# Optimization experiments

Measured on AMD Instinct MI355X. Metric: run time of the kernel, lower is better.

Reference implementation:

```python
import jax, jax.numpy as jnp
import numpy as np

N_NODES = 100000
N_EDGES = 1600000
N_AGENTS = 50000
D_X, D_LSTM, D_Z, D_EDGE = 64, 64, 32, 48
D_IN = D_X + D_LSTM + D_Z + D_EDGE  # 208
D_HID, D_OUT = 256, 64


def setup_inputs() -> dict:
    key = jax.random.key(0)
    ks = jax.random.split(key, 10)
    x = jax.random.normal(ks[0], (N_NODES, D_X), dtype=jnp.float32)
    x_lstm = jax.random.normal(ks[1], (N_AGENTS, D_LSTM), dtype=jnp.float32)
    encoded_z_gnss = jax.random.normal(ks[2], (N_AGENTS, D_Z), dtype=jnp.float32)
    edge_index = jax.random.randint(ks[3], (2, N_EDGES), 0, N_NODES, dtype=jnp.int64)
    edge_attr = jax.random.normal(ks[4], (N_EDGES, D_EDGE), dtype=jnp.float32)
    node_idx = jax.random.randint(ks[5], (N_AGENTS,), 0, N_NODES, dtype=jnp.int64)
    # MLP params (node_mlp: Linear(208,256) -> ReLU -> Linear(256,64))
    W1 = jax.random.normal(ks[6], (D_IN, D_HID), dtype=jnp.float32) * (1.0 / np.sqrt(D_IN))
    b1 = jnp.zeros((D_HID,), dtype=jnp.float32)
    W2 = jax.random.normal(ks[7], (D_HID, D_OUT), dtype=jnp.float32) * (1.0 / np.sqrt(D_HID))
    b2 = jnp.zeros((D_OUT,), dtype=jnp.float32)
    return {"x": x, "x_lstm": x_lstm, "encoded_z_gnss": encoded_z_gnss,
            "edge_index": edge_index, "edge_attr": edge_attr,
            "node_indexes_related_to_agent": node_idx,
            "W1": W1, "b1": b1, "W2": W2, "b2": b2}


def reference(x, x_lstm, encoded_z_gnss, edge_index, edge_attr,
              node_indexes_related_to_agent, W1, b1, W2, b2):
    row = edge_index[0]
    # node_agg_fn: scatter-sum edge features into source nodes -> [N, D_EDGE]
    agg = jax.ops.segment_sum(edge_attr, row, num_segments=x.shape[0])
    idx = node_indexes_related_to_agent
    # gather + concat -> [A, D_IN]
    out = jnp.concatenate([x[idx], x_lstm, encoded_z_gnss, agg[idx]], axis=1)
    # node_mlp
    h = jax.nn.relu(out @ W1 + b1)
    return h @ W2 + b2
```

## Files before the change

### kernel.cpp

```cpp
#include <hip/hip_runtime.h>

#define N_NODES  100000
#define N_EDGES  1600000
#define N_AGENTS 50000
#define D_EDGE   48
#define D_IN     208
#define D_HID    256
#define D_OUT    64

#define K1_PAD   224
#define F_STRIDE 248
#define H_STRIDE 264
#define AGB      64

#define BCAP     64

typedef __attribute__((ext_vector_type(8))) short short8;
typedef __attribute__((ext_vector_type(4))) float f32x4;

static __device__ __forceinline__ unsigned short f2bf(float f) {
    unsigned u = __float_as_uint(f);
    u += 0x7FFFu + ((u >> 16) & 1u);
    return (unsigned short)(u >> 16);
}

__global__ __launch_bounds__(256)
void prep_w(const float* __restrict__ W1, const float* __restrict__ W2,
            unsigned short* __restrict__ w1p, unsigned short* __restrict__ w2p) {
    int t = blockIdx.x * 256 + threadIdx.x;
    if (t < 16 * 7 * 64) {
        int lane = t & 63;
        int ks   = (t >> 6) % 7;
        int tile = t / (7 * 64);
        int n = tile * 16 + (lane & 15);
        int kb = ks * 32 + (lane >> 4) * 8;
        unsigned short v[8];
        #pragma unroll
        for (int j = 0; j < 8; ++j) {
            int k = kb + j;
            v[j] = (k < D_IN) ? f2bf(W1[k * D_HID + n]) : (unsigned short)0;
        }
        #pragma unroll
        for (int j = 0; j < 8; ++j) w1p[t * 8 + j] = v[j];
    } else if (t < 16 * 7 * 64 + 4 * 8 * 64) {
        int u = t - 16 * 7 * 64;
        int lane = u & 63;
        int ks   = (u >> 6) & 7;
        int tile = u / (8 * 64);
        int o = tile * 16 + (lane & 15);
        int kb = ks * 32 + (lane >> 4) * 8;
        #pragma unroll
        for (int j = 0; j < 8; ++j)
            w2p[u * 8 + j] = f2bf(W2[(kb + j) * D_OUT + o]);
    }
}

__global__ __launch_bounds__(256)
void mask_kernel(const int* __restrict__ node_idx, int* __restrict__ mask) {
    int i = blockIdx.x * 256 + threadIdx.x;
    if (i < N_AGENTS) mask[node_idx[i]] = 1;
}

__global__ __launch_bounds__(256)
void place_kernel(const int* __restrict__ row, const int* __restrict__ mask,
                  int* __restrict__ cnt, int* __restrict__ bucket) {
    int e = blockIdx.x * 256 + threadIdx.x;
    if (e >= N_EDGES) return;
    int r = row[e];
    if (!mask[r]) return;
    int pos = atomicAdd(&cnt[r], 1);
    if (pos < BCAP) bucket[r * BCAP + pos] = e;
}

__global__ __launch_bounds__(256)
void gather_kernel(const float* __restrict__ edge_attr,
                   const int* __restrict__ mask, const int* __restrict__ cnt,
                   const int* __restrict__ bucket,
                   float* __restrict__ agg) {
    int gid = blockIdx.x * 256 + threadIdx.x;
    if (gid >= N_NODES * D_EDGE) return;
    int n = gid / D_EDGE;
    int c = gid - n * D_EDGE;
    if (!mask[n]) return;
    int deg = cnt[n];
    if (deg > BCAP) deg = BCAP;
    const int* brow = &bucket[n * BCAP];
    float acc = 0.f;
    int j = 0;
    for (; j + 4 <= deg; j += 4) {
        int e0 = brow[j + 0];
        int e1 = brow[j + 1];
        int e2 = brow[j + 2];
        int e3 = brow[j + 3];
        float a0 = edge_attr[(long long)e0 * D_EDGE + c];
        float a1 = edge_attr[(long long)e1 * D_EDGE + c];
        float a2 = edge_attr[(long long)e2 * D_EDGE + c];
        float a3 = edge_attr[(long long)e3 * D_EDGE + c];
        acc += (a0 + a1) + (a2 + a3);
    }
    for (; j < deg; ++j) {
        int e0 = brow[j];
        acc += edge_attr[(long long)e0 * D_EDGE + c];
    }
    agg[(long long)n * D_EDGE + c] = acc;
}

__global__ __launch_bounds__(256)
void mlp_mfma(const float* __restrict__ x,
              const float* __restrict__ x_lstm,
              const float* __restrict__ z,
              const float* __restrict__ agg,
              const int* __restrict__ node_idx,
              const unsigned short* __restrict__ w1p,
              const float* __restrict__ b1,
              const unsigned short* __restrict__ w2p,
              const float* __restrict__ b2,
              float* __restrict__ out) {
    __shared__ unsigned short feat[AGB][F_STRIDE];
    __shared__ unsigned short hbuf[AGB][H_STRIDE];

    const int tid  = threadIdx.x;
    const int w    = tid >> 6;
    const int lane = tid & 63;
    const int ag0  = blockIdx.x * AGB;

    {
        const int a   = tid >> 2;
        const int sub = tid & 3;
        const int ag  = ag0 + a;
        unsigned short* frow = &feat[a][0];
        if (ag < N_AGENTS) {
            const int nid = node_idx[ag];
            #pragma unroll
            for (int i = 0; i < 4; ++i) {
                int q = i * 4 + sub;
                float4 v = *reinterpret_cast<const float4*>(&x[(long long)nid * 64 + q * 4]);
                ushort4 b; b.x = f2bf(v.x); b.y = f2bf(v.y); b.z = f2bf(v.z); b.w = f2bf(v.w);
                *reinterpret_cast<ushort4*>(&frow[q * 4]) = b;
            }
            #pragma unroll
            for (int i = 0; i < 4; ++i) {
                int q = i * 4 + sub;
                float4 v = *reinterpret_cast<const float4*>(&x_lstm[(long long)ag * 64 + q * 4]);
                ushort4 b; b.x = f2bf(v.x); b.y = f2bf(v.y); b.z = f2bf(v.z); b.w = f2bf(v.w);
                *reinterpret_cast<ushort4*>(&frow[64 + q * 4]) = b;
            }
            #pragma unroll
            for (int i = 0; i < 2; ++i) {
                int q = i * 4 + sub;
                float4 v = *reinterpret_cast<const float4*>(&z[(long long)ag * 32 + q * 4]);
                ushort4 b; b.x = f2bf(v.x); b.y = f2bf(v.y); b.z = f2bf(v.z); b.w = f2bf(v.w);
                *reinterpret_cast<ushort4*>(&frow[128 + q * 4]) = b;
            }
            #pragma unroll
            for (int i = 0; i < 3; ++i) {
                int q = i * 4 + sub;
                float4 v = *reinterpret_cast<const float4*>(&agg[(long long)nid * D_EDGE + q * 4]);
                ushort4 b; b.x = f2bf(v.x); b.y = f2bf(v.y); b.z = f2bf(v.z); b.w = f2bf(v.w);
                *reinterpret_cast<ushort4*>(&frow[160 + q * 4]) = b;
            }
            ushort4 zz; zz.x = 0; zz.y = 0; zz.z = 0; zz.w = 0;
            *reinterpret_cast<ushort4*>(&frow[208 + sub * 4]) = zz;
        } else {
            ushort4 zz; zz.x = 0; zz.y = 0; zz.z = 0; zz.w = 0;
            #pragma unroll
            for (int i = 0; i < 14; ++i)
                *reinterpret_cast<ushort4*>(&frow[(i * 4 + sub) * 4]) = zz;
        }
    }
    __syncthreads();

    const int m16 = lane & 15;
    const int g   = lane >> 4;

    const short8* w1v = reinterpret_cast<const short8*>(w1p);
    const short8* w2v = reinterpret_cast<const short8*>(w2p);

    for (int mc = 0; mc < 2; ++mc) {
        const int a0 = mc * 32 + m16;
        const int a1 = mc * 32 + 16 + m16;
        short8 bf0[7], bf1[7];
        #pragma unroll
        for (int ks = 0; ks < 7; ++ks) {
            bf0[ks] = *reinterpret_cast<const short8*>(&feat[a0][ks * 32 + g * 8]);
            bf1[ks] = *reinterpret_cast<const short8*>(&feat[a1][ks * 32 + g * 8]);
        }
        #pragma unroll
        for (int nt = 0; nt < 4; ++nt) {
            const int gt = w * 4 + nt;
            f32x4 c0 = {0.f, 0.f, 0.f, 0.f};
            f32x4 c1 = {0.f, 0.f, 0.f, 0.f};
            #pragma unroll
            for (int ks = 0; ks < 7; ++ks) {
                short8 wf = w1v[(gt * 7 + ks) * 64 + lane];
                c0 = __builtin_amdgcn_mfma_f32_16x16x32_bf16(wf, bf0[ks], c0, 0, 0, 0);
                c1 = __builtin_amdgcn_mfma_f32_16x16x32_bf16(wf, bf1[ks], c1, 0, 0, 0);
            }
            float4 bb = *reinterpret_cast<const float4*>(&b1[gt * 16 + g * 4]);
            ushort4 h0, h1;
            h0.x = f2bf(fmaxf(c0[0] + bb.x, 0.f));
            h0.y = f2bf(fmaxf(c0[1] + bb.y, 0.f));
            h0.z = f2bf(fmaxf(c0[2] + bb.z, 0.f));
            h0.w = f2bf(fmaxf(c0[3] + bb.w, 0.f));
            h1.x = f2bf(fmaxf(c1[0] + bb.x, 0.f));
            h1.y = f2bf(fmaxf(c1[1] + bb.y, 0.f));
            h1.z = f2bf(fmaxf(c1[2] + bb.z, 0.f));
            h1.w = f2bf(fmaxf(c1[3] + bb.w, 0.f));
            *reinterpret_cast<ushort4*>(&hbuf[a0][gt * 16 + g * 4]) = h0;
            *reinterpret_cast<ushort4*>(&hbuf[a1][gt * 16 + g * 4]) = h1;
        }
    }
    __syncthreads();

    {
        short8 w2f[8];
        #pragma unroll
        for (int ks = 0; ks < 8; ++ks)
            w2f[ks] = w2v[(w * 8 + ks) * 64 + lane];

        float4 bo = *reinterpret_cast<const float4*>(&b2[w * 16 + g * 4]);
        #pragma unroll
        for (int mt = 0; mt < 4; ++mt) {
            const int a = mt * 16 + m16;
            short8 hf[8];
            #pragma unroll
            for (int ks = 0; ks < 8; ++ks)
                hf[ks] = *reinterpret_cast<const short8*>(&hbuf[a][ks * 32 + g * 8]);
            f32x4 acc = {0.f, 0.f, 0.f, 0.f};
            #pragma unroll
            for (int ks = 0; ks < 8; ++ks)
                acc = __builtin_amdgcn_mfma_f32_16x16x32_bf16(w2f[ks], hf[ks], acc, 0, 0, 0);
            const int ag = ag0 + a;
            if (ag < N_AGENTS) {
                float4 o4;
                o4.x = acc[0] + bo.x;
                o4.y = acc[1] + bo.y;
                o4.z = acc[2] + bo.z;
                o4.w = acc[3] + bo.w;
                *reinterpret_cast<float4*>(&out[(long long)ag * D_OUT + w * 16 + g * 4]) = o4;
            }
        }
    }
}

extern "C" void kernel_launch(void* const* d_in, const int* in_sizes, int n_in,
                              void* d_out, int out_size, void* d_ws, size_t ws_size,
                              hipStream_t stream) {
    const float* x        = (const float*)d_in[0];
    const float* x_lstm   = (const float*)d_in[1];
    const float* z        = (const float*)d_in[2];
    const int*   edge_idx = (const int*)d_in[3];
    const float* edge_attr= (const float*)d_in[4];
    const int*   node_idx = (const int*)d_in[5];
    const float* W1       = (const float*)d_in[6];
    const float* b1       = (const float*)d_in[7];
    const float* W2       = (const float*)d_in[8];
    const float* b2       = (const float*)d_in[9];
    float* out = (float*)d_out;

    char* wsp = (char*)d_ws;
    size_t o = 0;
    auto alloc = [&](size_t bytes) { char* p = wsp + o; o = (o + bytes + 255) & ~(size_t)255; return p; };
    float* agg  = (float*)alloc((size_t)N_NODES * D_EDGE * 4);
    int* cnt    = (int*)alloc((size_t)N_NODES * 4);
    int* mask   = (int*)alloc((size_t)N_NODES * 4);
    int* bucket = (int*)alloc((size_t)N_NODES * BCAP * 4);
    unsigned short* w1p = (unsigned short*)alloc((size_t)16 * 7 * 64 * 8 * 2);
    unsigned short* w2p = (unsigned short*)alloc((size_t)4 * 8 * 64 * 8 * 2);

    hipMemsetAsync(cnt, 0, (size_t)((char*)bucket - (char*)cnt), stream);

    prep_w<<<(16 * 7 * 64 + 4 * 8 * 64 + 255) / 256, 256, 0, stream>>>(W1, W2, w1p, w2p);
    mask_kernel<<<(N_AGENTS + 255) / 256, 256, 0, stream>>>(node_idx, mask);
    place_kernel<<<(N_EDGES + 255) / 256, 256, 0, stream>>>(edge_idx, mask, cnt, bucket);
    gather_kernel<<<(N_NODES * D_EDGE + 255) / 256, 256, 0, stream>>>(
        edge_attr, mask, cnt, bucket, agg);
    mlp_mfma<<<(N_AGENTS + AGB - 1) / AGB, 256, 0, stream>>>(x, x_lstm, z, agg, node_idx,
                                                             w1p, b1, w2p, b2, out);
}
```

Before: 114.6 us.

## Fuse edge aggregation into MLP kernel and merge memset into weight prep

Drops the separate gather kernel and the agg buffer. Each agent's feature-load threads now sum their node's bucketed edge rows directly, with float4 loads, before converting to bf16. The hipMemsetAsync of cnt and mask is folded into the weight-prep kernel as extra zeroing blocks, which removes a launch and the agg write/read round trip. The cost is more irregular gather work inside the MLP kernel, and duplicate node indices now redo the same aggregation.

```diff
diff --git a/kernel.cpp b/kernel.cpp
--- a/kernel.cpp
+++ b/kernel.cpp
@@ -14,6 +14,8 @@
 #define AGB      64
 
 #define BCAP     64
+#define PREP_BLOCKS 36
+#define ZERO_INT4   50016
 
 typedef __attribute__((ext_vector_type(8))) short short8;
 typedef __attribute__((ext_vector_type(4))) float f32x4;
@@ -25,33 +27,43 @@
 }
 
 __global__ __launch_bounds__(256)
-void prep_w(const float* __restrict__ W1, const float* __restrict__ W2,
-            unsigned short* __restrict__ w1p, unsigned short* __restrict__ w2p) {
-    int t = blockIdx.x * 256 + threadIdx.x;
-    if (t < 16 * 7 * 64) {
-        int lane = t & 63;
-        int ks   = (t >> 6) % 7;
-        int tile = t / (7 * 64);
-        int n = tile * 16 + (lane & 15);
-        int kb = ks * 32 + (lane >> 4) * 8;
-        unsigned short v[8];
-        #pragma unroll
-        for (int j = 0; j < 8; ++j) {
-            int k = kb + j;
-            v[j] = (k < D_IN) ? f2bf(W1[k * D_HID + n]) : (unsigned short)0;
-        }
-        #pragma unroll
-        for (int j = 0; j < 8; ++j) w1p[t * 8 + j] = v[j];
-    } else if (t < 16 * 7 * 64 + 4 * 8 * 64) {
-        int u = t - 16 * 7 * 64;
-        int lane = u & 63;
-        int ks   = (u >> 6) & 7;
-        int tile = u / (8 * 64);
-        int o = tile * 16 + (lane & 15);
-        int kb = ks * 32 + (lane >> 4) * 8;
-        #pragma unroll
-        for (int j = 0; j < 8; ++j)
-            w2p[u * 8 + j] = f2bf(W2[(kb + j) * D_OUT + o]);
+void prep0(const float* __restrict__ W1, const float* __restrict__ W2,
+           unsigned short* __restrict__ w1p, unsigned short* __restrict__ w2p,
+           int4* __restrict__ zbase) {
+    const int b = blockIdx.x;
+    if (b < PREP_BLOCKS) {
+        int t = b * 256 + threadIdx.x;
+        if (t < 16 * 7 * 64) {
+            int lane = t & 63;
+            int ks   = (t >> 6) % 7;
+            int tile = t / (7 * 64);
+            int n = tile * 16 + (lane & 15);
+            int kb = ks * 32 + (lane >> 4) * 8;
+            unsigned short v[8];
+            #pragma unroll
+            for (int j = 0; j < 8; ++j) {
+                int k = kb + j;
+                v[j] = (k < D_IN) ? f2bf(W1[k * D_HID + n]) : (unsigned short)0;
+            }
+            #pragma unroll
+            for (int j = 0; j < 8; ++j) w1p[t * 8 + j] = v[j];
+        } else if (t < 16 * 7 * 64 + 4 * 8 * 64) {
+            int u = t - 16 * 7 * 64;
+            int lane = u & 63;
+            int ks   = (u >> 6) & 7;
+            int tile = u / (8 * 64);
+            int o = tile * 16 + (lane & 15);
+            int kb = ks * 32 + (lane >> 4) * 8;
+            #pragma unroll
+            for (int j = 0; j < 8; ++j)
+                w2p[u * 8 + j] = f2bf(W2[(kb + j) * D_OUT + o]);
+        }
+    } else {
+        int i = (b - PREP_BLOCKS) * 256 + threadIdx.x;
+        if (i < ZERO_INT4) {
+            int4 zz; zz.x = 0; zz.y = 0; zz.z = 0; zz.w = 0;
+            zbase[i] = zz;
+        }
     }
 }
 
@@ -69,47 +81,16 @@
     int r = row[e];
     if (!mask[r]) return;
     int pos = atomicAdd(&cnt[r], 1);
-    if (pos < BCAP) bucket[r * BCAP + pos] = e;
-}
-
-__global__ __launch_bounds__(256)
-void gather_kernel(const float* __restrict__ edge_attr,
-                   const int* __restrict__ mask, const int* __restrict__ cnt,
-                   const int* __restrict__ bucket,
-                   float* __restrict__ agg) {
-    int gid = blockIdx.x * 256 + threadIdx.x;
-    if (gid >= N_NODES * D_EDGE) return;
-    int n = gid / D_EDGE;
-    int c = gid - n * D_EDGE;
-    if (!mask[n]) return;
-    int deg = cnt[n];
-    if (deg > BCAP) deg = BCAP;
-    const int* brow = &bucket[n * BCAP];
-    float acc = 0.f;
-    int j = 0;
-    for (; j + 4 <= deg; j += 4) {
-        int e0 = brow[j + 0];
-        int e1 = brow[j + 1];
-        int e2 = brow[j + 2];
-        int e3 = brow[j + 3];
-        float a0 = edge_attr[(long long)e0 * D_EDGE + c];
-        float a1 = edge_attr[(long long)e1 * D_EDGE + c];
-        float a2 = edge_attr[(long long)e2 * D_EDGE + c];
-        float a3 = edge_attr[(long long)e3 * D_EDGE + c];
-        acc += (a0 + a1) + (a2 + a3);
-    }
-    for (; j < deg; ++j) {
-        int e0 = brow[j];
-        acc += edge_attr[(long long)e0 * D_EDGE + c];
-    }
-    agg[(long long)n * D_EDGE + c] = acc;
+    if ((unsigned)pos < (unsigned)BCAP) bucket[r * BCAP + pos] = e;
 }
 
 __global__ __launch_bounds__(256)
 void mlp_mfma(const float* __restrict__ x,
               const float* __restrict__ x_lstm,
               const float* __restrict__ z,
-              const float* __restrict__ agg,
+              const float* __restrict__ edge_attr,
+              const int* __restrict__ cnt,
+              const int* __restrict__ bucket,
               const int* __restrict__ node_idx,
               const unsigned short* __restrict__ w1p,
               const float* __restrict__ b1,
@@ -152,12 +133,47 @@
                 ushort4 b; b.x = f2bf(v.x); b.y = f2bf(v.y); b.z = f2bf(v.z); b.w = f2bf(v.w);
                 *reinterpret_cast<ushort4*>(&frow[128 + q * 4]) = b;
             }
-            #pragma unroll
-            for (int i = 0; i < 3; ++i) {
-                int q = i * 4 + sub;
-                float4 v = *reinterpret_cast<const float4*>(&agg[(long long)nid * D_EDGE + q * 4]);
-                ushort4 b; b.x = f2bf(v.x); b.y = f2bf(v.y); b.z = f2bf(v.z); b.w = f2bf(v.w);
-                *reinterpret_cast<ushort4*>(&frow[160 + q * 4]) = b;
+            {
+                int deg = cnt[nid];
+                if (deg > BCAP) deg = BCAP;
+                const int* brow = &bucket[nid * BCAP];
+                const float* ea = edge_attr + sub * 12;
+                float acc[12];
+                #pragma unroll
+                for (int q = 0; q < 12; ++q) acc[q] = 0.f;
+                int j = 0;
+                for (; j + 2 <= deg; j += 2) {
+                    const float* p0 = ea + (long long)brow[j] * D_EDGE;
+                    const float* p1 = ea + (long long)brow[j + 1] * D_EDGE;
+                    float4 a0 = *reinterpret_cast<const float4*>(p0);
+                    float4 a1 = *reinterpret_cast<const float4*>(p0 + 4);
+                    float4 a2 = *reinterpret_cast<const float4*>(p0 + 8);
+                    float4 c0 = *reinterpret_cast<const float4*>(p1);
+                    float4 c1 = *reinterpret_cast<const float4*>(p1 + 4);
+                    float4 c2 = *reinterpret_cast<const float4*>(p1 + 8);
+                    acc[0] += a0.x; acc[1] += a0.y; acc[2]  += a0.z; acc[3]  += a0.w;
+                    acc[4] += a1.x; acc[5] += a1.y; acc[6]  += a1.z; acc[7]  += a1.w;
+                    acc[8] += a2.x; acc[9] += a2.y; acc[10] += a2.z; acc[11] += a2.w;
+                    acc[0] += c0.x; acc[1] += c0.y; acc[2]  += c0.z; acc[3]  += c0.w;
+                    acc[4] += c1.x; acc[5] += c1.y; acc[6]  += c1.z; acc[7]  += c1.w;
+                    acc[8] += c2.x; acc[9] += c2.y; acc[10] += c2.z; acc[11] += c2.w;
+                }
+                if (j < deg) {
+                    const float* p0 = ea + (long long)brow[j] * D_EDGE;
+                    float4 a0 = *reinterpret_cast<const float4*>(p0);
+                    float4 a1 = *reinterpret_cast<const float4*>(p0 + 4);
+                    float4 a2 = *reinterpret_cast<const float4*>(p0 + 8);
+                    acc[0] += a0.x; acc[1] += a0.y; acc[2]  += a0.z; acc[3]  += a0.w;
+                    acc[4] += a1.x; acc[5] += a1.y; acc[6]  += a1.z; acc[7]  += a1.w;
+                    acc[8] += a2.x; acc[9] += a2.y; acc[10] += a2.z; acc[11] += a2.w;
+                }
+                ushort4 u0, u1, u2;
+                u0.x = f2bf(acc[0]); u0.y = f2bf(acc[1]); u0.z = f2bf(acc[2]);  u0.w = f2bf(acc[3]);
+                u1.x = f2bf(acc[4]); u1.y = f2bf(acc[5]); u1.z = f2bf(acc[6]);  u1.w = f2bf(acc[7]);
+                u2.x = f2bf(acc[8]); u2.y = f2bf(acc[9]); u2.z = f2bf(acc[10]); u2.w = f2bf(acc[11]);
+                *reinterpret_cast<ushort4*>(&frow[160 + sub * 12])     = u0;
+                *reinterpret_cast<ushort4*>(&frow[160 + sub * 12 + 4]) = u1;
+                *reinterpret_cast<ushort4*>(&frow[160 + sub * 12 + 8]) = u2;
             }
             ushort4 zz; zz.x = 0; zz.y = 0; zz.z = 0; zz.w = 0;
             *reinterpret_cast<ushort4*>(&frow[208 + sub * 4]) = zz;
@@ -261,20 +277,16 @@
     char* wsp = (char*)d_ws;
     size_t o = 0;
     auto alloc = [&](size_t bytes) { char* p = wsp + o; o = (o + bytes + 255) & ~(size_t)255; return p; };
-    float* agg  = (float*)alloc((size_t)N_NODES * D_EDGE * 4);
     int* cnt    = (int*)alloc((size_t)N_NODES * 4);
     int* mask   = (int*)alloc((size_t)N_NODES * 4);
     int* bucket = (int*)alloc((size_t)N_NODES * BCAP * 4);
     unsigned short* w1p = (unsigned short*)alloc((size_t)16 * 7 * 64 * 8 * 2);
     unsigned short* w2p = (unsigned short*)alloc((size_t)4 * 8 * 64 * 8 * 2);
 
-    hipMemsetAsync(cnt, 0, (size_t)((char*)bucket - (char*)cnt), stream);
-
-    prep_w<<<(16 * 7 * 64 + 4 * 8 * 64 + 255) / 256, 256, 0, stream>>>(W1, W2, w1p, w2p);
+    prep0<<<PREP_BLOCKS + (ZERO_INT4 + 255) / 256, 256, 0, stream>>>(
+        W1, W2, w1p, w2p, (int4*)cnt);
     mask_kernel<<<(N_AGENTS + 255) / 256, 256, 0, stream>>>(node_idx, mask);
     place_kernel<<<(N_EDGES + 255) / 256, 256, 0, stream>>>(edge_idx, mask, cnt, bucket);
-    gather_kernel<<<(N_NODES * D_EDGE + 255) / 256, 256, 0, stream>>>(
-        edge_attr, mask, cnt, bucket, agg);
-    mlp_mfma<<<(N_AGENTS + AGB - 1) / AGB, 256, 0, stream>>>(x, x_lstm, z, agg, node_idx,
-                                                             w1p, b1, w2p, b2, out);
-}
+    mlp_mfma<<<(N_AGENTS + AGB - 1) / AGB, 256, 0, stream>>>(
+        x, x_lstm, z, edge_attr, cnt, bucket, node_idx, w1p, b1, w2p, b2, out);
+}
```

After: 99.27 us. -13.4%, faster.
